# Performance work log

Hardware: AMD Instinct MI355X
Metric: run time of the kernel (lower is better)

## Reference

```python
import jax, jax.numpy as jnp
import numpy as np

# Static config (init_kwargs)
H = 56; W = 56; C = 256; NH = 8; WS = 7; SS = 3
HD = C // NH
SCALE = HD ** -0.5
N = WS * WS                      # tokens per window = 49
NW = (H // WS) * (W // WS)       # windows per image = 64
HIDDEN = int(C * 4.0)
EPS = 1e-5


def _rel_pos_index():
    coords = np.stack(np.meshgrid(np.arange(WS), np.arange(WS), indexing='ij')).reshape(2, -1)
    rel = coords[:, :, None] - coords[:, None, :]          # [2, N, N]
    rel = rel.transpose(1, 2, 0).astype(np.int64)          # [N, N, 2]
    rel[:, :, 0] += WS - 1
    rel[:, :, 1] += WS - 1
    rel[:, :, 0] *= 2 * WS - 1
    return rel.sum(-1).reshape(-1)                         # [N*N]


def _attn_mask():
    # (0 / -100) mask for the shifted-window configuration, [NW, N, N]
    img = np.zeros([H, W])
    cnt = 0
    for hs in (slice(0, -WS), slice(-WS, -SS), slice(-SS, None)):
        for ws in (slice(0, -WS), slice(-WS, -SS), slice(-SS, None)):
            img[hs, ws] = cnt
            cnt += 1
    mw = img.reshape(H // WS, WS, W // WS, WS).transpose(0, 2, 1, 3).reshape(-1, N)
    diff = mw[:, None, :] - mw[:, :, None]                 # [NW, N, N]
    return np.where(diff != 0, -100.0, 0.0).astype(np.float32)


_REL_IDX = _rel_pos_index()
_MASK = _attn_mask()


def _ln(x, g, b):
    mu = jnp.mean(x, axis=-1, keepdims=True)
    var = jnp.mean((x - mu) ** 2, axis=-1, keepdims=True)
    return (x - mu) * jax.lax.rsqrt(var + EPS) * g + b


def setup_inputs() -> dict:
    key = jax.random.key(0)
    ks = jax.random.split(key, 16)
    B = 32
    s = 0.02
    return {
        'x': jax.random.normal(ks[0], (B, H * W, C), dtype=jnp.float32),
        'gamma1': jnp.ones((C,), jnp.float32),
        'beta1': jnp.zeros((C,), jnp.float32),
        'qkv_w': jax.random.normal(ks[1], (C, 3 * C), jnp.float32) * s,
        'qkv_b': jnp.zeros((3 * C,), jnp.float32),
        'proj_w': jax.random.normal(ks[2], (C, C), jnp.float32) * s,
        'proj_b': jnp.zeros((C,), jnp.float32),
        'rpb_table': jax.random.normal(ks[3], ((2 * WS - 1) * (2 * WS - 1), NH), jnp.float32) * s,
        'gamma2': jnp.ones((C,), jnp.float32),
        'beta2': jnp.zeros((C,), jnp.float32),
        'fc1_w': jax.random.normal(ks[4], (C, HIDDEN), jnp.float32) * s,
        'fc1_b': jnp.zeros((HIDDEN,), jnp.float32),
        'fc2_w': jax.random.normal(ks[5], (HIDDEN, C), jnp.float32) * s,
        'fc2_b': jnp.zeros((C,), jnp.float32),
    }


def reference(x, gamma1, beta1, qkv_w, qkv_b, proj_w, proj_b, rpb_table,
              gamma2, beta2, fc1_w, fc1_b, fc2_w, fc2_b):
    B = x.shape[0]
    y = _ln(x, gamma1, beta1).reshape(B, H, W, C)
    # cyclic shift
    y = jnp.roll(y, (-SS, -SS), axis=(1, 2))
    # window partition -> [B*NW, N, C]
    win = y.reshape(B, H // WS, WS, W // WS, WS, C)
    win = win.transpose(0, 1, 3, 2, 4, 5).reshape(-1, N, C)
    # qkv projection, split heads
    qkv = (win @ qkv_w + qkv_b).reshape(-1, N, 3, NH, HD).transpose(2, 0, 3, 1, 4)
    q, k, v = qkv[0] * SCALE, qkv[1], qkv[2]            # [B*NW, NH, N, HD]
    attn = jnp.einsum('bhnd,bhmd->bhnm', q, k)          # [B*NW, NH, N, N]
    # gathered relative position bias
    bias = rpb_table[jnp.asarray(_REL_IDX)].reshape(N, N, NH).transpose(2, 0, 1)
    attn = attn + bias[None]
    # shift mask
    mask = jnp.asarray(_MASK)                           # [NW, N, N]
    attn = attn.reshape(B, NW, NH, N, N) + mask[None, :, None]
    attn = jax.nn.softmax(attn.reshape(-1, NH, N, N), axis=-1)
    o = jnp.einsum('bhnm,bhmd->bnhd', attn, v).reshape(-1, N, C)
    o = o @ proj_w + proj_b
    # window reverse + reverse shift
    o = o.reshape(B, H // WS, W // WS, WS, WS, C).transpose(0, 1, 3, 2, 4, 5).reshape(B, H, W, C)
    o = jnp.roll(o, (SS, SS), axis=(1, 2)).reshape(B, H * W, C)
    x = x + o
    # MLP block
    y = _ln(x, gamma2, beta2)
    y = jax.nn.gelu(y @ fc1_w + fc1_b, approximate=False) @ fc2_w + fc2_b
    return x + y
```

## Files before the change

### kernel.cpp

```cpp
#include <hip/hip_runtime.h>
#include <hip/hip_bf16.h>
#include <math.h>


typedef __bf16 bf16_t;
typedef __bf16 bf16x4 __attribute__((ext_vector_type(4)));
typedef __bf16 bf16x8 __attribute__((ext_vector_type(8)));
typedef float f32x4 __attribute__((ext_vector_type(4)));

#define AS1 __attribute__((address_space(1)))
#define AS3 __attribute__((address_space(3)))

__device__ __forceinline__ void gload_lds16(const bf16_t* g, bf16_t* l) {
  __builtin_amdgcn_global_load_lds((AS1 void*)g, (AS3 void*)l, 16, 0, 0);
}

__global__ void transpose_cast3(const float* __restrict__ qkv_w,
                                const float* __restrict__ proj_w,
                                const float* __restrict__ fc1_w,
                                bf16_t* __restrict__ qkvWt,
                                bf16_t* __restrict__ projWt,
                                bf16_t* __restrict__ fc1Wt) {
  int idx = blockIdx.x * 256 + threadIdx.x;
  const float* w;
  bf16_t* wt;
  int N;
  if (blockIdx.y == 0) { w = qkv_w; wt = qkvWt; N = 768; }
  else if (blockIdx.y == 1) { w = proj_w; wt = projWt; N = 256; }
  else { w = fc1_w; wt = fc1Wt; N = 1024; }
  if (idx < N * 256) {
    int n = idx >> 8, k = idx & 255;
    wt[idx] = (bf16_t)w[(size_t)k * N + n];
  }
}

__global__ void transpose_cast(const float* __restrict__ w, bf16_t* __restrict__ wt,
                               int K, int N) {
  int idx = blockIdx.x * 256 + threadIdx.x;
  if (idx < N * K) {
    int n = idx / K, k = idx - n * K;
    wt[idx] = (bf16_t)w[(size_t)k * N + n];
  }
}

__global__ void build_bm(const float* __restrict__ rpb, float* __restrict__ bm) {
  int t = blockIdx.x, h = blockIdx.y;
  int wr = (t & 2) ? 7 : 0, wc = (t & 1) ? 7 : 0;
  for (int e = threadIdx.x; e < 4096; e += 256) {
    int r = e >> 6, c = e & 63;
    float v;
    if (c >= 49) {
      v = -30000.f;
    } else if (r >= 49) {
      v = 0.f;
    } else {
      int r1 = r / 7, c1 = r - r1 * 7;
      int r2 = c / 7, c2 = c - r2 * 7;
      v = rpb[((r1 - r2 + 6) * 13 + (c1 - c2 + 6)) * 8 + h];
      int hp = wr * 7 + r1, wp = wc * 7 + c1;
      int hq = wr * 7 + r2, wq = wc * 7 + c2;
      int ri = (hp < 49 ? 0 : (hp < 53 ? 1 : 2)) * 3 + (wp < 49 ? 0 : (wp < 53 ? 1 : 2));
      int rj = (hq < 49 ? 0 : (hq < 53 ? 1 : 2)) * 3 + (wq < 49 ? 0 : (wq < 53 ? 1 : 2));
      if (ri != rj) v -= 100.f;
    }
    bm[((size_t)(t * 8 + h) * 64 + r) * 64 + c] = v;
  }
}

__global__ __launch_bounds__(256)
void ln_cast(const float* __restrict__ src, const float* __restrict__ gamma,
             const float* __restrict__ beta, bf16_t* __restrict__ dst, int windowed) {
  int row = blockIdx.x * 4 + (threadIdx.x >> 6);
  int lane = threadIdx.x & 63;
  size_t srow;
  if (windowed) {
    int w = row / 49, t = row - w * 49;
    int img = w >> 6, wi = w & 63;
    int wr = wi >> 3, wc = wi & 7;
    int rr = t / 7, cc = t - rr * 7;
    int h = wr * 7 + rr + 3; if (h >= 56) h -= 56;
    int ww = wc * 7 + cc + 3; if (ww >= 56) ww -= 56;
    srow = (size_t)img * 3136 + h * 56 + ww;
  } else {
    srow = row;
  }
  float4 v = *(const float4*)(src + srow * 256 + lane * 4);
  float s = v.x + v.y + v.z + v.w;
  float s2 = v.x * v.x + v.y * v.y + v.z * v.z + v.w * v.w;
#pragma unroll
  for (int off = 32; off > 0; off >>= 1) {
    s += __shfl_xor(s, off);
    s2 += __shfl_xor(s2, off);
  }
  float mu = s * (1.0f / 256.0f);
  float rs = rsqrtf(s2 * (1.0f / 256.0f) - mu * mu + 1e-5f);
  float4 g = *(const float4*)(gamma + lane * 4);
  float4 b = *(const float4*)(beta + lane * 4);
  bf16x4 o;
  o[0] = (bf16_t)((v.x - mu) * rs * g.x + b.x);
  o[1] = (bf16_t)((v.y - mu) * rs * g.y + b.y);
  o[2] = (bf16_t)((v.z - mu) * rs * g.z + b.z);
  o[3] = (bf16_t)((v.w - mu) * rs * g.w + b.w);
  *(bf16x4*)(dst + (size_t)row * 256 + lane * 4) = o;
}

template <int MODE>
__global__ __launch_bounds__(256)
void gemm_bt(const bf16_t* __restrict__ A, const bf16_t* __restrict__ Bt,
             const float* __restrict__ bias,
             bf16_t* Cbf, float* Cf, const float* Res,
             int M, int N, int K, int nblk) {
  __shared__ __align__(16) bf16_t As[128 * 32];
  __shared__ __align__(16) bf16_t Bs[128 * 32];
  const int tid = threadIdx.x;
  const int lane = tid & 63;
  const int wave = tid >> 6;
  const int wm = wave & 1, wn = wave >> 1;
  const int bid = blockIdx.x;
  const int m_idx = bid / nblk;
  const int n_idx = bid - m_idx * nblk;
  const int m0 = m_idx * 128;
  const int n0 = n_idx * 128;

  f32x4 acc[4][4];
#pragma unroll
  for (int i = 0; i < 4; i++)
#pragma unroll
    for (int j = 0; j < 4; j++) acc[i][j] = f32x4{0.f, 0.f, 0.f, 0.f};

  const bf16_t* Ag = A + (size_t)m0 * K;
  const bf16_t* Bg = Bt + (size_t)n0 * K;
  const int lr = lane & 15;
  const int kq = (lane >> 4) * 8;

  for (int k0 = 0; k0 < K; k0 += 32) {
#pragma unroll
    for (int it = 0; it < 2; it++) {
      int slot = it * 256 + tid;
      int row = slot >> 2;
      int ko = (slot & 3) << 3;
      bf16_t* ldsA = As + (it * 256 + wave * 64) * 8;
      bf16_t* ldsB = Bs + (it * 256 + wave * 64) * 8;
      gload_lds16(Ag + (size_t)row * K + k0 + ko, ldsA);
      gload_lds16(Bg + (size_t)row * K + k0 + ko, ldsB);
    }
    __syncthreads();
    bf16x8 af[4], bfr[4];
#pragma unroll
    for (int i = 0; i < 4; i++) {
      af[i]  = *(const bf16x8*)(As + (wm * 64 + i * 16 + lr) * 32 + kq);
      bfr[i] = *(const bf16x8*)(Bs + (wn * 64 + i * 16 + lr) * 32 + kq);
    }
#pragma unroll
    for (int i = 0; i < 4; i++)
#pragma unroll
      for (int j = 0; j < 4; j++)
        acc[i][j] = __builtin_amdgcn_mfma_f32_16x16x32_bf16(af[i], bfr[j], acc[i][j], 0, 0, 0);
    __syncthreads();
  }

  const int quad = lane >> 4;
#pragma unroll
  for (int i = 0; i < 4; i++) {
    int rbase = m0 + wm * 64 + i * 16 + quad * 4;
#pragma unroll
    for (int j = 0; j < 4; j++) {
      int col = n0 + wn * 64 + j * 16 + lr;
      float bi = bias[col];
#pragma unroll
      for (int r = 0; r < 4; r++) {
        int row = rbase + r;
        float v = acc[i][j][r] + bi;
        if (MODE == 0) {
          Cbf[(size_t)row * N + col] = (bf16_t)v;
        } else {
          int w = row / 49, t = row - w * 49;
          int img = w >> 6, wi = w & 63;
          int wr = wi >> 3, wc = wi & 7;
          int rr = t / 7, cc = t - rr * 7;
          int h = wr * 7 + rr + 3; if (h >= 56) h -= 56;
          int ww2 = wc * 7 + cc + 3; if (ww2 >= 56) ww2 -= 56;
          size_t idx = ((size_t)img * 3136 + h * 56 + ww2) * 256 + col;
          Cf[idx] = v + Res[idx];
        }
      }
    }
  }
}

__global__ __launch_bounds__(256)
void attn_mfma(const bf16_t* __restrict__ qkv, const float* __restrict__ bm,
               bf16_t* __restrict__ o) {
  __shared__ __align__(16) bf16_t Ps[64 * 72];
  __shared__ __align__(16) bf16_t Vt[32 * 72];
  const int w = blockIdx.x, h = blockIdx.y;
  const int tid = threadIdx.x;
  const int lane = tid & 63, wv = tid >> 6;
  const int lr = lane & 15, quad = lane >> 4;
  const int wi = w & 63;
  const int mtype = (((wi >> 3) == 7) ? 2 : 0) | (((wi & 7) == 7) ? 1 : 0);
  const bf16_t* base = qkv + (size_t)w * 49 * 768 + h * 32;

  bf16x8 zero8;
#pragma unroll
  for (int z = 0; z < 8; z++) zero8[z] = (bf16_t)0.f;

  {
    int tok = tid >> 2, d8 = (tid & 3) * 8;
    bf16x8 v8 = zero8;
    if (tok < 49) v8 = *(const bf16x8*)(base + (size_t)tok * 768 + 512 + d8);
#pragma unroll
    for (int z = 0; z < 8; z++) Vt[(d8 + z) * 72 + tok] = v8[z];
  }
  __syncthreads();

  const int mrow = 16 * wv + lr;
  bf16x8 aq = zero8;
  if (mrow < 49) aq = *(const bf16x8*)(base + (size_t)mrow * 768 + quad * 8);
  f32x4 s[4];
#pragma unroll
  for (int j = 0; j < 4; j++) {
    int nrow = 16 * j + lr;
    bf16x8 bk = zero8;
    if (nrow < 49) bk = *(const bf16x8*)(base + (size_t)nrow * 768 + 256 + quad * 8);
    s[j] = __builtin_amdgcn_mfma_f32_16x16x32_bf16(aq, bk, f32x4{0.f, 0.f, 0.f, 0.f}, 0, 0, 0);
  }

  const float* bmb = bm + ((size_t)(mtype * 8 + h) * 64 + 16 * wv) * 64;
  float inv[4];
#pragma unroll
  for (int reg = 0; reg < 4; reg++) {
    int rl = quad * 4 + reg;
    float v0[4];
    float mx = -1e30f;
#pragma unroll
    for (int j = 0; j < 4; j++) {
      float v = s[j][reg] * 0.17677669529663689f + bmb[rl * 64 + 16 * j + lr];
      v0[j] = v;
      mx = fmaxf(mx, v);
    }
#pragma unroll
    for (int off = 8; off > 0; off >>= 1) mx = fmaxf(mx, __shfl_xor(mx, off));
    float sum = 0.f;
#pragma unroll
    for (int j = 0; j < 4; j++) {
      float e = __expf(v0[j] - mx);
      v0[j] = e;
      sum += e;
    }
#pragma unroll
    for (int off = 8; off > 0; off >>= 1) sum += __shfl_xor(sum, off);
    inv[reg] = 1.0f / sum;
#pragma unroll
    for (int j = 0; j < 4; j++)
      Ps[(16 * wv + rl) * 72 + 16 * j + lr] = (bf16_t)v0[j];
  }

  f32x4 oacc[2];
  oacc[0] = f32x4{0.f, 0.f, 0.f, 0.f};
  oacc[1] = f32x4{0.f, 0.f, 0.f, 0.f};
#pragma unroll
  for (int kk = 0; kk < 2; kk++) {
    bf16x8 ap = *(const bf16x8*)(Ps + (16 * wv + lr) * 72 + kk * 32 + quad * 8);
#pragma unroll
    for (int n = 0; n < 2; n++) {
      bf16x8 bv = *(const bf16x8*)(Vt + (16 * n + lr) * 72 + kk * 32 + quad * 8);
      oacc[n] = __builtin_amdgcn_mfma_f32_16x16x32_bf16(ap, bv, oacc[n], 0, 0, 0);
    }
  }
#pragma unroll
  for (int n = 0; n < 2; n++) {
#pragma unroll
    for (int reg = 0; reg < 4; reg++) {
      int row = 16 * wv + quad * 4 + reg;
      if (row < 49) {
        int d = 16 * n + lr;
        o[((size_t)w * 49 + row) * 256 + h * 32 + d] = (bf16_t)(oacc[n][reg] * inv[reg]);
      }
    }
  }
}

__global__ __launch_bounds__(256, 2)
void fused_mlp(const bf16_t* __restrict__ y2, const bf16_t* __restrict__ W1t,
               const float* __restrict__ b1, const bf16_t* __restrict__ W2t,
               const float* __restrict__ b2, float* __restrict__ out) {
  __shared__ __align__(16) bf16_t Ws[3 * 8192];
  __shared__ __align__(16) bf16_t Hs[4 * 16 * 136];
  __shared__ float b1s[1024];
  const int tid = threadIdx.x;
  const int lane = tid & 63, wave = tid >> 6;
  const int lr = lane & 15, quad = lane >> 4;
  const int m0 = blockIdx.x * 64;
  bf16_t* HsW = Hs + wave * (16 * 136);

  for (int i = tid; i < 1024; i += 256) b1s[i] = b1[i];

  const bf16_t* Arow = y2 + (size_t)(m0 + 16 * wave + lr) * 256;
  bf16x8 aF[2][4];
#pragma unroll
  for (int ks = 0; ks < 2; ks++)
#pragma unroll
    for (int kk = 0; kk < 4; kk++)
      aF[ks][kk] = *(const bf16x8*)(Arow + ks * 128 + kk * 32 + quad * 8);

  f32x4 acc2[16];
#pragma unroll
  for (int n = 0; n < 16; n++) acc2[n] = f32x4{0.f, 0.f, 0.f, 0.f};

  const int rowA = wave * 8 + (lane >> 3);
  const int koffA = ((((lane & 7) << 4) ^ ((lane >> 3) << 4)) >> 1);
  const int rowB = wave * 16 + (lane >> 2);
  const int koffB = ((((lane & 3) << 4) ^ (((lane >> 2) & 3) << 4)) >> 1);
  const int swzA = (lr & 7) << 4;
  const int swzB = (lr & 3) << 4;

  auto issue = [&](int s2, int buf) {
    int hc2 = s2 >> 3, sub2 = s2 & 3;
    bf16_t* dst = Ws + buf * 8192;
    if (((s2 >> 2) & 1) == 0) {
#pragma unroll
      for (int it = 0; it < 4; it++)
        gload_lds16(W1t + (size_t)(hc2 * 128 + it * 32 + rowA) * 256 + sub2 * 64 + koffA,
                    dst + it * 2048 + wave * 512);
    } else {
#pragma unroll
      for (int it = 0; it < 4; it++)
        gload_lds16(W2t + (size_t)(it * 64 + rowB) * 1024 + hc2 * 128 + sub2 * 32 + koffB,
                    dst + it * 2048 + wave * 512);
    }
  };

  asm volatile("s_waitcnt vmcnt(0) lgkmcnt(0)" ::: "memory");
  issue(0, 0);
  issue(1, 1);
  int cur = 0, nxt = 1, nx2 = 2;

  for (int hc = 0; hc < 8; hc++) {
    f32x4 acc1[8];
#pragma unroll
    for (int j = 0; j < 8; j++) acc1[j] = f32x4{0.f, 0.f, 0.f, 0.f};

#pragma unroll
    for (int sub = 0; sub < 4; sub++) {
      const int s = hc * 8 + sub;
      if (s + 2 < 64) issue(s + 2, nx2);
      if (s < 62)       asm volatile("s_waitcnt vmcnt(8)" ::: "memory");
      else if (s == 62) asm volatile("s_waitcnt vmcnt(4)" ::: "memory");
      else              asm volatile("s_waitcnt vmcnt(0)" ::: "memory");
      __builtin_amdgcn_s_barrier();
      __builtin_amdgcn_sched_barrier(0);
      const char* WsC = (const char*)(Ws + cur * 8192);
#pragma unroll
      for (int kk2 = 0; kk2 < 2; kk2++) {
        bf16x8 aa = aF[sub >> 1][(sub & 1) * 2 + kk2];
#pragma unroll
        for (int j = 0; j < 8; j++) {
          bf16x8 b = *(const bf16x8*)(WsC + (16 * j + lr) * 128 +
                                      ((kk2 * 64 + quad * 16) ^ swzA));
          acc1[j] = __builtin_amdgcn_mfma_f32_16x16x32_bf16(aa, b, acc1[j], 0, 0, 0);
        }
      }
      asm volatile("s_waitcnt lgkmcnt(0)" ::: "memory");
      __builtin_amdgcn_sched_barrier(0);
      __builtin_amdgcn_s_barrier();
      int t = cur; cur = nxt; nxt = nx2; nx2 = t;
    }

#pragma unroll
    for (int j = 0; j < 8; j++) {
      float bias1 = b1s[hc * 128 + 16 * j + lr];
#pragma unroll
      for (int reg = 0; reg < 4; reg++) {
        float v = acc1[j][reg] + bias1;
        v = 0.5f * v * (1.0f + erff(v * 0.70710678118654752f));
        HsW[(4 * quad + reg) * 136 + 16 * j + lr] = (bf16_t)v;
      }
    }

#pragma unroll
    for (int sub = 0; sub < 4; sub++) {
      const int s = hc * 8 + 4 + sub;
      if (s + 2 < 64) issue(s + 2, nx2);
      if (s < 62)       asm volatile("s_waitcnt vmcnt(8)" ::: "memory");
      else if (s == 62) asm volatile("s_waitcnt vmcnt(4)" ::: "memory");
      else              asm volatile("s_waitcnt vmcnt(0)" ::: "memory");
      __builtin_amdgcn_s_barrier();
      __builtin_amdgcn_sched_barrier(0);
      const char* WsC = (const char*)(Ws + cur * 8192);
      bf16x8 ah = *(const bf16x8*)(HsW + lr * 136 + sub * 32 + quad * 8);
#pragma unroll
      for (int n = 0; n < 16; n++) {
        bf16x8 bw = *(const bf16x8*)(WsC + (16 * n + lr) * 64 +
                                     ((quad * 16) ^ swzB));
        acc2[n] = __builtin_amdgcn_mfma_f32_16x16x32_bf16(ah, bw, acc2[n], 0, 0, 0);
      }
      asm volatile("s_waitcnt lgkmcnt(0)" ::: "memory");
      __builtin_amdgcn_sched_barrier(0);
      __builtin_amdgcn_s_barrier();
      int t = cur; cur = nxt; nxt = nx2; nx2 = t;
    }
  }

#pragma unroll
  for (int n = 0; n < 16; n++) {
    int col = 16 * n + lr;
    float bi = b2[col];
#pragma unroll
    for (int reg = 0; reg < 4; reg++) {
      int row = m0 + 16 * wave + 4 * quad + reg;
      size_t idx = (size_t)row * 256 + col;
      out[idx] = acc2[n][reg] + bi + out[idx];
    }
  }
}

extern "C" void kernel_launch(void* const* d_in, const int* in_sizes, int n_in,
                              void* d_out, int out_size, void* d_ws, size_t ws_size,
                              hipStream_t stream) {
  const float* x      = (const float*)d_in[0];
  const float* g1     = (const float*)d_in[1];
  const float* b1     = (const float*)d_in[2];
  const float* qkv_w  = (const float*)d_in[3];
  const float* qkv_b  = (const float*)d_in[4];
  const float* proj_w = (const float*)d_in[5];
  const float* proj_b = (const float*)d_in[6];
  const float* rpb    = (const float*)d_in[7];
  const float* g2     = (const float*)d_in[8];
  const float* b2     = (const float*)d_in[9];
  const float* fc1_w  = (const float*)d_in[10];
  const float* fc1_b  = (const float*)d_in[11];
  const float* fc2_w  = (const float*)d_in[12];
  const float* fc2_b  = (const float*)d_in[13];
  float* out = (float*)d_out;
  char* ws = (char*)d_ws;

  bf16_t* xw   = (bf16_t*)ws;
  bf16_t* qkv  = (bf16_t*)(ws + 51380224);
  bf16_t* ow   = (bf16_t*)(ws + 205520896);
  bf16_t* y2   = xw;
  bf16_t* qkvWt  = (bf16_t*)(ws + 256901120);
  bf16_t* projWt = qkvWt + 768 * 256;
  bf16_t* fc1Wt  = projWt + 256 * 256;
  bf16_t* fc2Wt  = fc1Wt + 1024 * 256;
  float*  bm     = (float*)fc2Wt;

  transpose_cast3<<<dim3(1024, 3), 256, 0, stream>>>(qkv_w, proj_w, fc1_w,
                                                     qkvWt, projWt, fc1Wt);
  build_bm<<<dim3(4, 8), 256, 0, stream>>>(rpb, bm);

  ln_cast<<<25088, 256, 0, stream>>>(x, g1, b1, xw, 1);
  gemm_bt<0><<<784 * 6, 256, 0, stream>>>(xw, qkvWt, qkv_b, qkv, nullptr, nullptr,
                                          100352, 768, 256, 6);
  attn_mfma<<<dim3(2048, 8), 256, 0, stream>>>(qkv, bm, ow);
  transpose_cast<<<(256 * 1024 + 255) / 256, 256, 0, stream>>>(fc2_w, fc2Wt, 1024, 256);
  gemm_bt<3><<<784 * 2, 256, 0, stream>>>(ow, projWt, proj_b, nullptr, out, x,
                                          100352, 256, 256, 2);
  ln_cast<<<25088, 256, 0, stream>>>(out, g2, b2, y2, 0);
  fused_mlp<<<1568, 256, 0, stream>>>(y2, fc1Wt, fc1_b, fc2Wt, fc2_b, out);
}
```

Before: 806.9 us.

## Restructure fused MLP weight pipeline to double-buffering and raise occupancy

The fused MLP kernel drops from a triple-buffered weight staging ring with hand-tuned vmcnt waits to a simpler double-buffered scheme, guarded by __syncthreads. Each step prefetches the next weight tile right after the barrier. This shrinks LDS use and also drops the b1 LDS staging, so launch bounds can allow 3 blocks per CU instead of 2. s_setprio is raised around the MFMA loops. The trade is a shallower prefetch depth and full barriers that wait for all outstanding loads, in exchange for more resident waves to hide latency.

```diff
diff --git a/kernel.cpp b/kernel.cpp
--- a/kernel.cpp
+++ b/kernel.cpp
@@ -281,60 +281,49 @@
   }
 }
 
-__global__ __launch_bounds__(256, 2)
+__global__ __launch_bounds__(256, 3)
 void fused_mlp(const bf16_t* __restrict__ y2, const bf16_t* __restrict__ W1t,
                const float* __restrict__ b1, const bf16_t* __restrict__ W2t,
                const float* __restrict__ b2, float* __restrict__ out) {
-  __shared__ __align__(16) bf16_t Ws[3 * 8192];
+  __shared__ __align__(16) bf16_t Ws[2 * 8192];
   __shared__ __align__(16) bf16_t Hs[4 * 16 * 136];
-  __shared__ float b1s[1024];
   const int tid = threadIdx.x;
   const int lane = tid & 63, wave = tid >> 6;
   const int lr = lane & 15, quad = lane >> 4;
   const int m0 = blockIdx.x * 64;
   bf16_t* HsW = Hs + wave * (16 * 136);
 
-  for (int i = tid; i < 1024; i += 256) b1s[i] = b1[i];
-
   const bf16_t* Arow = y2 + (size_t)(m0 + 16 * wave + lr) * 256;
-  bf16x8 aF[2][4];
-#pragma unroll
-  for (int ks = 0; ks < 2; ks++)
-#pragma unroll
-    for (int kk = 0; kk < 4; kk++)
-      aF[ks][kk] = *(const bf16x8*)(Arow + ks * 128 + kk * 32 + quad * 8);
+  bf16x8 aFf[8];
+#pragma unroll
+  for (int i = 0; i < 8; i++)
+    aFf[i] = *(const bf16x8*)(Arow + i * 32 + quad * 8);
 
   f32x4 acc2[16];
 #pragma unroll
   for (int n = 0; n < 16; n++) acc2[n] = f32x4{0.f, 0.f, 0.f, 0.f};
 
   const int rowA = wave * 8 + (lane >> 3);
-  const int koffA = ((((lane & 7) << 4) ^ ((lane >> 3) << 4)) >> 1);
+  const int koffA = ((((lane & 7) << 4) ^ (((lane >> 3) & 7) << 4)) >> 1);
   const int rowB = wave * 16 + (lane >> 2);
   const int koffB = ((((lane & 3) << 4) ^ (((lane >> 2) & 3) << 4)) >> 1);
   const int swzA = (lr & 7) << 4;
   const int swzB = (lr & 3) << 4;
 
-  auto issue = [&](int s2, int buf) {
-    int hc2 = s2 >> 3, sub2 = s2 & 3;
-    bf16_t* dst = Ws + buf * 8192;
-    if (((s2 >> 2) & 1) == 0) {
-#pragma unroll
-      for (int it = 0; it < 4; it++)
-        gload_lds16(W1t + (size_t)(hc2 * 128 + it * 32 + rowA) * 256 + sub2 * 64 + koffA,
-                    dst + it * 2048 + wave * 512);
-    } else {
-#pragma unroll
-      for (int it = 0; it < 4; it++)
-        gload_lds16(W2t + (size_t)(it * 64 + rowB) * 1024 + hc2 * 128 + sub2 * 32 + koffB,
-                    dst + it * 2048 + wave * 512);
-    }
+  auto issueA = [&](int hc2, int sub2, int buf) {
+#pragma unroll
+    for (int it = 0; it < 4; it++)
+      gload_lds16(W1t + (size_t)(hc2 * 128 + it * 32 + rowA) * 256 + sub2 * 64 + koffA,
+                  Ws + buf * 8192 + it * 2048 + wave * 512);
   };
-
-  asm volatile("s_waitcnt vmcnt(0) lgkmcnt(0)" ::: "memory");
-  issue(0, 0);
-  issue(1, 1);
-  int cur = 0, nxt = 1, nx2 = 2;
+  auto issueB = [&](int hc2, int sub2, int buf) {
+#pragma unroll
+    for (int it = 0; it < 4; it++)
+      gload_lds16(W2t + (size_t)(it * 64 + rowB) * 1024 + hc2 * 128 + sub2 * 32 + koffB,
+                  Ws + buf * 8192 + it * 2048 + wave * 512);
+  };
+
+  issueA(0, 0, 0);
 
   for (int hc = 0; hc < 8; hc++) {
     f32x4 acc1[8];
@@ -343,17 +332,14 @@
 
 #pragma unroll
     for (int sub = 0; sub < 4; sub++) {
-      const int s = hc * 8 + sub;
-      if (s + 2 < 64) issue(s + 2, nx2);
-      if (s < 62)       asm volatile("s_waitcnt vmcnt(8)" ::: "memory");
-      else if (s == 62) asm volatile("s_waitcnt vmcnt(4)" ::: "memory");
-      else              asm volatile("s_waitcnt vmcnt(0)" ::: "memory");
-      __builtin_amdgcn_s_barrier();
-      __builtin_amdgcn_sched_barrier(0);
-      const char* WsC = (const char*)(Ws + cur * 8192);
+      __syncthreads();
+      if (sub < 3) issueA(hc, sub + 1, (sub + 1) & 1);
+      else         issueB(hc, 0, (sub + 1) & 1);
+      const char* WsC = (const char*)(Ws + (sub & 1) * 8192);
+      __builtin_amdgcn_s_setprio(1);
 #pragma unroll
       for (int kk2 = 0; kk2 < 2; kk2++) {
-        bf16x8 aa = aF[sub >> 1][(sub & 1) * 2 + kk2];
+        bf16x8 aa = aFf[sub * 2 + kk2];
 #pragma unroll
         for (int j = 0; j < 8; j++) {
           bf16x8 b = *(const bf16x8*)(WsC + (16 * j + lr) * 128 +
@@ -361,44 +347,36 @@
           acc1[j] = __builtin_amdgcn_mfma_f32_16x16x32_bf16(aa, b, acc1[j], 0, 0, 0);
         }
       }
-      asm volatile("s_waitcnt lgkmcnt(0)" ::: "memory");
-      __builtin_amdgcn_sched_barrier(0);
-      __builtin_amdgcn_s_barrier();
-      int t = cur; cur = nxt; nxt = nx2; nx2 = t;
-    }
-
-#pragma unroll
-    for (int j = 0; j < 8; j++) {
-      float bias1 = b1s[hc * 128 + 16 * j + lr];
-#pragma unroll
-      for (int reg = 0; reg < 4; reg++) {
-        float v = acc1[j][reg] + bias1;
-        v = 0.5f * v * (1.0f + erff(v * 0.70710678118654752f));
-        HsW[(4 * quad + reg) * 136 + 16 * j + lr] = (bf16_t)v;
+      __builtin_amdgcn_s_setprio(0);
+      if (sub == 3) {
+#pragma unroll
+        for (int j = 0; j < 8; j++) {
+          float bias1 = b1[hc * 128 + 16 * j + lr];
+#pragma unroll
+          for (int reg = 0; reg < 4; reg++) {
+            float v = acc1[j][reg] + bias1;
+            v = 0.5f * v * (1.0f + erff(v * 0.70710678118654752f));
+            HsW[(4 * quad + reg) * 136 + 16 * j + lr] = (bf16_t)v;
+          }
+        }
       }
     }
 
 #pragma unroll
     for (int sub = 0; sub < 4; sub++) {
-      const int s = hc * 8 + 4 + sub;
-      if (s + 2 < 64) issue(s + 2, nx2);
-      if (s < 62)       asm volatile("s_waitcnt vmcnt(8)" ::: "memory");
-      else if (s == 62) asm volatile("s_waitcnt vmcnt(4)" ::: "memory");
-      else              asm volatile("s_waitcnt vmcnt(0)" ::: "memory");
-      __builtin_amdgcn_s_barrier();
-      __builtin_amdgcn_sched_barrier(0);
-      const char* WsC = (const char*)(Ws + cur * 8192);
+      __syncthreads();
+      if (sub < 3)      issueB(hc, sub + 1, (sub + 1) & 1);
+      else if (hc < 7)  issueA(hc + 1, 0, (sub + 1) & 1);
+      const char* WsC = (const char*)(Ws + (sub & 1) * 8192);
       bf16x8 ah = *(const bf16x8*)(HsW + lr * 136 + sub * 32 + quad * 8);
+      __builtin_amdgcn_s_setprio(1);
 #pragma unroll
       for (int n = 0; n < 16; n++) {
         bf16x8 bw = *(const bf16x8*)(WsC + (16 * n + lr) * 64 +
                                      ((quad * 16) ^ swzB));
         acc2[n] = __builtin_amdgcn_mfma_f32_16x16x32_bf16(ah, bw, acc2[n], 0, 0, 0);
       }
-      asm volatile("s_waitcnt lgkmcnt(0)" ::: "memory");
-      __builtin_amdgcn_sched_barrier(0);
-      __builtin_amdgcn_s_barrier();
-      int t = cur; cur = nxt; nxt = nx2; nx2 = t;
+      __builtin_amdgcn_s_setprio(0);
     }
   }
 
```

Measured after the change: 794.6 us. Within noise of the previous version (-1.5%).
